# Performance work log

Hardware: AMD Instinct MI355X
Metric: run time of the kernel (lower is better)

## Reference

```python
import jax, jax.numpy as jnp
import numpy as np

B, C, T = 64, 22, 2560
U0, U1 = 128, 64  # lstm units per direction


def _lstm(x, Wx, Wh, b, reverse):
    """Keras-style LSTM. x:[B,T,D]. Returns (seq:[B,T,U], last:[B,U])."""
    if reverse:
        x = x[:, ::-1, :]
    U = Wh.shape[0]
    # precompute input projections for all timesteps: [T,B,4U]
    xz = (jnp.einsum('btd,dk->btk', x, Wx) + b).transpose(1, 0, 2)
    h0 = jnp.zeros((x.shape[0], U), x.dtype)
    c0 = jnp.zeros((x.shape[0], U), x.dtype)

    def step(carry, z):
        h, c = carry
        z = z + h @ Wh
        i = jax.nn.sigmoid(z[:, :U])
        f = jax.nn.sigmoid(z[:, U:2 * U])
        g = jnp.tanh(z[:, 2 * U:3 * U])
        o = jax.nn.sigmoid(z[:, 3 * U:])
        c = f * c + i * g
        h = o * jnp.tanh(c)
        return (h, c), h

    (h_last, _), hs = jax.lax.scan(step, (h0, c0), xz)
    hs = hs.transpose(1, 0, 2)  # [B,T,U]
    if reverse:
        hs = hs[:, ::-1, :]
    return hs, h_last


def setup_inputs() -> dict:
    key = jax.random.key(0)
    ks = jax.random.split(key, 20)
    s = 0.05
    d = {"x": jax.random.normal(ks[0], (B, C, T), jnp.float32)}
    # layer 0 (input dim C=22, units U0), fwd + bwd
    d["l0f_Wx"] = jax.random.normal(ks[1], (C, 4 * U0)) * s
    d["l0f_Wh"] = jax.random.normal(ks[2], (U0, 4 * U0)) * s
    d["l0f_b"] = jnp.zeros((4 * U0,))
    d["l0b_Wx"] = jax.random.normal(ks[3], (C, 4 * U0)) * s
    d["l0b_Wh"] = jax.random.normal(ks[4], (U0, 4 * U0)) * s
    d["l0b_b"] = jnp.zeros((4 * U0,))
    # layer 1 (input dim 2*U0=256, units U1), fwd + bwd
    d["l1f_Wx"] = jax.random.normal(ks[5], (2 * U0, 4 * U1)) * s
    d["l1f_Wh"] = jax.random.normal(ks[6], (U1, 4 * U1)) * s
    d["l1f_b"] = jnp.zeros((4 * U1,))
    d["l1b_Wx"] = jax.random.normal(ks[7], (2 * U0, 4 * U1)) * s
    d["l1b_Wh"] = jax.random.normal(ks[8], (U1, 4 * U1)) * s
    d["l1b_b"] = jnp.zeros((4 * U1,))
    # dense head: 2*U1=128 -> 128 -> 64 -> 1
    d["d0_W"] = jax.random.normal(ks[9], (2 * U1, 128)) * s
    d["d0_b"] = jnp.zeros((128,))
    d["d1_W"] = jax.random.normal(ks[10], (128, 64)) * s
    d["d1_b"] = jnp.zeros((64,))
    d["out_W"] = jax.random.normal(ks[11], (64, 1)) * s
    d["out_b"] = jnp.zeros((1,))
    return d


def reference(x, l0f_Wx, l0f_Wh, l0f_b, l0b_Wx, l0b_Wh, l0b_b,
              l1f_Wx, l1f_Wh, l1f_b, l1b_Wx, l1b_Wh, l1b_b,
              d0_W, d0_b, d1_W, d1_b, out_W, out_b):
    h = x.transpose(0, 2, 1)  # [B,T,C]
    # BiLSTM 0, return_sequences=True
    f_seq, _ = _lstm(h, l0f_Wx, l0f_Wh, l0f_b, reverse=False)
    b_seq, _ = _lstm(h, l0b_Wx, l0b_Wh, l0b_b, reverse=True)
    h = jnp.concatenate([f_seq, b_seq], axis=-1)  # [B,T,2*U0]
    # BiLSTM 1, return last state
    _, f_last = _lstm(h, l1f_Wx, l1f_Wh, l1f_b, reverse=False)
    _, b_last = _lstm(h, l1b_Wx, l1b_Wh, l1b_b, reverse=True)
    h = jnp.concatenate([f_last, b_last], axis=-1)  # [B,2*U1]
    # dense head (dropout inactive at inference)
    h = jax.nn.relu(h @ d0_W + d0_b)
    h = jax.nn.relu(h @ d1_W + d1_b)
    return jax.nn.sigmoid(h @ out_W + out_b)  # [B,1]
```

## Files before the change

kernel.cpp:

```cpp
#include <hip/hip_runtime.h>
#include <stdint.h>

#define TT 2560
#define BB 64
#define CC 22

typedef unsigned short ushort_t;
typedef __attribute__((ext_vector_type(4))) float floatx4;
typedef __attribute__((ext_vector_type(8))) short bf16x8;
typedef __attribute__((ext_vector_type(4))) int intx4;

__device__ __forceinline__ float bf2f(ushort_t u){
  union { uint32_t i; float f; } v; v.i = ((uint32_t)u) << 16; return v.f;
}
__device__ __forceinline__ ushort_t f2bf(float f){
  union { float f; uint32_t i; } v; v.f = f;
  uint32_t r = v.i + 0x7FFFu + ((v.i >> 16) & 1u);
  return (ushort_t)(r >> 16);
}
__device__ __forceinline__ float fsig(float x){ return 1.f/(1.f + __expf(-x)); }
__device__ __forceinline__ float ftanh(float x){ return 2.f/(1.f + __expf(-2.f*x)) - 1.f; }

__device__ __forceinline__ void ldsbar(){
  asm volatile("s_waitcnt lgkmcnt(0)\n\ts_barrier" ::: "memory");
}

__global__ __launch_bounds__(256) void k_convert_x(const float* __restrict__ x, ushort_t* __restrict__ xc){
  int i4 = blockIdx.x*256 + threadIdx.x;
  if (i4 >= BB*CC*TT/4) return;
  const float4 v = ((const float4*)x)[i4];
  uint2 o;
  o.x = (uint32_t)f2bf(v.x) | ((uint32_t)f2bf(v.y) << 16);
  o.y = (uint32_t)f2bf(v.z) | ((uint32_t)f2bf(v.w) << 16);
  ((uint2*)xc)[i4] = o;
}

__global__ __launch_bounds__(256) void k_prep_xa(const ushort_t* __restrict__ xc, ushort_t* __restrict__ xA){
  int idx = blockIdx.x*256 + threadIdx.x;
  if (idx >= BB*TT*4) return;
  int q = idx & 3;
  int rest = idx >> 2;
  int t = rest % TT, b = rest / TT;
  ushort_t v[8];
  #pragma unroll
  for (int j=0;j<8;j++){
    int c = q*8 + j;
    v[j] = (c < CC) ? xc[((size_t)b*CC + c)*TT + t] : (ushort_t)0;
  }
  *(uint4*)(xA + (size_t)idx*8) = *(const uint4*)v;
}

__global__ __launch_bounds__(256) void k_wmax(const float* __restrict__ w0f, const float* __restrict__ w0b,
                                              const float* __restrict__ w1f, const float* __restrict__ w1b,
                                              float* __restrict__ scl){
  const int b = blockIdx.x;
  const float* W = (b==0) ? w0f : (b==1) ? w0b : (b==2) ? w1f : w1b;
  const int n = (b < 2) ? 128*512 : 64*256;
  float mx = 0.f;
  for (int i = threadIdx.x; i < n; i += 256) mx = fmaxf(mx, fabsf(W[i]));
  __shared__ float red[256];
  red[threadIdx.x] = mx;
  __syncthreads();
  for (int s = 128; s > 0; s >>= 1){
    if (threadIdx.x < s) red[threadIdx.x] = fmaxf(red[threadIdx.x], red[threadIdx.x+s]);
    __syncthreads();
  }
  if (threadIdx.x == 0) scl[b] = fmaxf(red[0], 1e-8f);
}

__global__ __launch_bounds__(256) void k_prep_l0(const float* __restrict__ WxF, const float* __restrict__ WhF,
                                                 const float* __restrict__ WxB, const float* __restrict__ WhB,
                                                 const float* __restrict__ scl,
                                                 char* __restrict__ W0Q, ushort_t* __restrict__ B0X){
  int idx = blockIdx.x*256 + threadIdx.x;
  if (idx >= 2*512*160) return;
  int dir = idx / 81920; int r0 = idx % 81920; int n = r0 / 160; int k = r0 % 160;
  int g = n >> 7, u = n & 127;
  int wv = u >> 4, qq = (u >> 2) & 3, r = u & 3;
  int row = (qq*8 + wv)*16 + (r*4 + g);
  if (k < 128){
    const float* Wh = dir ? WhB : WhF;
    float sw = scl[dir];
    W0Q[(size_t)dir*65536 + row*128 + k] = (char)(int)rintf(Wh[k*512 + n] * (127.f/sw));
  } else {
    const float* Wx = dir ? WxB : WxF;
    int kx = k - 128;
    float v = (kx < CC) ? Wx[kx*512 + n] : 0.f;
    B0X[(size_t)dir*16384 + row*32 + kx] = f2bf(v);
  }
}

__global__ __launch_bounds__(256) void k_prep_l1(const float* __restrict__ WhF, const float* __restrict__ WhB,
                                                 const float* __restrict__ scl,
                                                 char* __restrict__ W1Q){
  int idx = blockIdx.x*256 + threadIdx.x;
  if (idx >= 2*256*64) return;
  int dir = idx >> 14; int r = idx & 16383; int n = r >> 6; int k = r & 63;
  const float* Wh = dir ? WhB : WhF;
  float sw = scl[2+dir];
  W1Q[(size_t)dir*16384 + n*64 + k] = (char)(int)rintf(Wh[k*256 + n] * (127.f/sw));
}

__global__ __launch_bounds__(256) void k_prep_wxT(const float* __restrict__ Wf, const float* __restrict__ Wb,
                                                  ushort_t* __restrict__ WT){
  int idx = blockIdx.x*256 + threadIdx.x;
  int dir = idx >> 16; int r = idx & 65535; int n = r >> 8; int k = r & 255;
  const float* W = dir ? Wb : Wf;
  WT[idx] = f2bf(W[k*256 + n]);
}

__global__ __launch_bounds__(512, 1) void k_lstm0m(
  const ushort_t* __restrict__ xA, const char* __restrict__ W0Q,
  const ushort_t* __restrict__ B0X, const float* __restrict__ scl,
  const float* __restrict__ bF, const float* __restrict__ bB,
  ushort_t* __restrict__ h0seq)
{
  const int dir = blockIdx.x & 1, b = blockIdx.x >> 1;
  const int tid = threadIdx.x;
  const int wv = tid >> 6, lane = tid & 63, m = lane & 15, q = lane >> 4;
  const int g  = m & 3;
  const int u  = wv*16 + q*4 + (m >> 2);
  const float* bi = dir ? bB : bF;
  const float sclc = scl[dir] * (1.f/16129.f);
  const float em = (g==2) ? -2.f : -1.f;
  const float ym = (g==2) ?  2.f :  1.f;
  const float ya = (g==2) ? -1.f :  0.f;
  const float bzl = bi[g*128 + u];

  __shared__ __align__(16) char AbufC[2][128];

  bf16x8 Bfx[4];
  intx4  BfQ[4][2];
  {
    const ushort_t* Bx = B0X + (size_t)dir*16384;
    const char*     Bq = W0Q + (size_t)dir*65536;
    #pragma unroll
    for (int qt=0; qt<4; qt++){
      int nrow = (qt*8 + wv)*16 + m;
      Bfx[qt] = *(const bf16x8*)(Bx + (size_t)nrow*32 + q*8);
      #pragma unroll
      for (int kt=0; kt<2; kt++)
        BfQ[qt][kt] = *(const intx4*)(Bq + (size_t)nrow*128 + kt*64 + q*16);
    }
  }

  if (tid < 64) ((uint32_t*)AbufC)[tid] = 0u;

  const ushort_t* xap = xA + ((size_t)b*TT*4 + q)*8;
  uint4 px[4];
  #pragma unroll
  for (int j=0; j<4; j++){
    int tj = dir ? (TT-1-j) : j;
    px[j] = *(const uint4*)(xap + (size_t)tj*32);
  }
  const ushort_t* xpp = xap + (size_t)(dir ? (TT-5) : 4)*32;
  const int xstep = dir ? -32 : 32;
  __syncthreads();

  const floatx4 z4 = {0.f,0.f,0.f,0.f};
  const intx4  zi = {0,0,0,0};
  float cst = 0.f;
  const int t00 = dir ? TT-1 : 0;
  ushort_t* hp = h0seq + ((size_t)b*TT + t00)*256 + dir*128 + u;
  const int hstep = dir ? -256 : 256;

  for (int i = 0; i < TT/4; ++i){
    #pragma unroll
    for (int p = 0; p < 4; ++p){
      const int s = i*4 + p;
      const int cur = s & 1, nxt = cur ^ 1;

      const char* ar = &AbufC[cur][0];
      intx4 AfQ0 = *(const intx4*)(ar + q*16);
      intx4 AfQ1 = *(const intx4*)(ar + 64 + q*16);
      bf16x8 Ax = *(const bf16x8*)&px[p];

      floatx4 ax0 = __builtin_amdgcn_mfma_f32_16x16x32_bf16(Ax, Bfx[0], z4, 0,0,0);
      floatx4 ax1 = __builtin_amdgcn_mfma_f32_16x16x32_bf16(Ax, Bfx[1], z4, 0,0,0);
      floatx4 ax2 = __builtin_amdgcn_mfma_f32_16x16x32_bf16(Ax, Bfx[2], z4, 0,0,0);
      floatx4 ax3 = __builtin_amdgcn_mfma_f32_16x16x32_bf16(Ax, Bfx[3], z4, 0,0,0);

      intx4 aq0 = __builtin_amdgcn_mfma_i32_16x16x64_i8(AfQ0, BfQ[0][0], zi, 0,0,0);
      intx4 aq1 = __builtin_amdgcn_mfma_i32_16x16x64_i8(AfQ0, BfQ[1][0], zi, 0,0,0);
      intx4 aq2 = __builtin_amdgcn_mfma_i32_16x16x64_i8(AfQ0, BfQ[2][0], zi, 0,0,0);
      intx4 aq3 = __builtin_amdgcn_mfma_i32_16x16x64_i8(AfQ0, BfQ[3][0], zi, 0,0,0);
      aq0 = __builtin_amdgcn_mfma_i32_16x16x64_i8(AfQ1, BfQ[0][1], aq0, 0,0,0);
      aq1 = __builtin_amdgcn_mfma_i32_16x16x64_i8(AfQ1, BfQ[1][1], aq1, 0,0,0);
      aq2 = __builtin_amdgcn_mfma_i32_16x16x64_i8(AfQ1, BfQ[2][1], aq2, 0,0,0);
      aq3 = __builtin_amdgcn_mfma_i32_16x16x64_i8(AfQ1, BfQ[3][1], aq3, 0,0,0);

      px[p] = *(const uint4*)xpp;
      xpp += xstep;

      float axs = (q < 2) ? ((q == 0) ? ax0[0] : ax1[0])
                          : ((q == 2) ? ax2[0] : ax3[0]);
      int   aqs = (q < 2) ? ((q == 0) ? aq0[0] : aq1[0])
                          : ((q == 2) ? aq2[0] : aq3[0]);

      {
        float z = (float)aqs*sclc + axs + bzl;
        float e = __expf(z * em);
        float y = 1.f/(1.f + e);
        float act = ym*y + ya;

        int ai = __float_as_int(act);
        float sf = __int_as_float(__builtin_amdgcn_ds_swizzle(ai, 0x041F));
        float sg = __int_as_float(__builtin_amdgcn_ds_swizzle(ai, 0x081F));
        float so = __int_as_float(__builtin_amdgcn_ds_swizzle(ai, 0x0C1F));

        float cc = sf*cst + act*sg;
        cst = cc;
        float hl = so*ftanh(cc);
        if (g == 0){
          AbufC[nxt][u] = (char)(int)rintf(hl * 127.f);
          *hp = f2bf(hl);
        }
        hp += hstep;
      }
      ldsbar();
    }
  }
}

__global__ __launch_bounds__(512) void k_xz1_gemm(const ushort_t* __restrict__ h0seq,
                                                  const ushort_t* __restrict__ WxT,
                                                  ushort_t* __restrict__ xz1)
{
  const int mb  = blockIdx.x;
  const int dir = blockIdx.y;
  const ushort_t* W   = WxT + (size_t)dir*256*256;
  ushort_t*       out = xz1 + (size_t)dir*BB*TT*256;
  const int wave = threadIdx.x >> 6;
  const int lane = threadIdx.x & 63;
  const int mw = wave & 3;
  const int nw = wave >> 2;
  const int m_ = lane & 15;
  const int q_ = lane >> 4;

  floatx4 acc[2][8];
  #pragma unroll
  for (int a=0;a<2;a++)
    #pragma unroll
    for (int n=0;n<8;n++) acc[a][n] = (floatx4)0.f;

  const size_t Abase = ((size_t)mb*128 + mw*32 + m_)*256 + q_*8;
  const size_t Bbase = ((size_t)nw*128 + m_)*256 + q_*8;

  for (int kc = 0; kc < 256; kc += 32){
    bf16x8 afr[2];
    #pragma unroll
    for (int mt=0;mt<2;mt++)
      afr[mt] = *(const bf16x8*)(h0seq + Abase + (size_t)mt*16*256 + kc);
    #pragma unroll
    for (int nt=0;nt<8;nt++){
      bf16x8 bfr = *(const bf16x8*)(W + Bbase + (size_t)nt*16*256 + kc);
      #pragma unroll
      for (int mt=0;mt<2;mt++)
        acc[mt][nt] = __builtin_amdgcn_mfma_f32_16x16x32_bf16(afr[mt], bfr, acc[mt][nt], 0,0,0);
    }
  }
  #pragma unroll
  for (int mt=0;mt<2;mt++)
    #pragma unroll
    for (int r=0;r<4;r++){
      size_t bt = (size_t)mb*128 + mw*32 + mt*16 + q_*4 + r;
      ushort_t* rowp = out + bt*256;
      #pragma unroll
      for (int wvz=0; wvz<4; wvz++){
        uint32_t lo = f2bf(acc[mt][wvz][r]);
        uint32_t hi = f2bf(acc[mt][wvz+4][r]);
        *(uint32_t*)(rowp + (wvz*16+m_)*4 + 2*nw) = lo | (hi << 16);
      }
    }
}

__global__ __launch_bounds__(256, 1) void k_lstm1m(
  const ushort_t* __restrict__ xz1R,
  const char* __restrict__ W1Q,
  const float* __restrict__ scl,
  const float* __restrict__ bF, const float* __restrict__ bB,
  float* __restrict__ h1last)
{
  const int dir = blockIdx.x & 1, cb = blockIdx.x >> 1;
  const int tid = threadIdx.x;
  const int wv = tid >> 6, lane = tid & 63, m = lane & 15, q = lane >> 4;
  const int u = wv*16 + m;
  const float* bi = dir ? bB : bF;
  const float sclc = scl[2+dir] * (1.f/16129.f);

  __shared__ __align__(16) char HbufC[2][4][80];

  intx4 BfQ[4];
  {
    const char* Bq = W1Q + (size_t)dir*16384;
    #pragma unroll
    for (int g=0; g<4; g++){
      int nrow = (g*4 + wv)*16 + m;
      BfQ[g] = *(const intx4*)(Bq + (size_t)nrow*64 + q*16);
    }
  }
  float bz[4];
  #pragma unroll
  for (int g=0; g<4; g++) bz[g] = bi[g*64 + u];

  if (tid < (int)(sizeof(HbufC)/4)) ((uint32_t*)HbufC)[tid] = 0u;

  const ushort_t* xzr = xz1R + ((size_t)dir*BB + (size_t)(cb*4+q))*TT*256 + (size_t)u*4;
  uint2 pz[4];
  #pragma unroll
  for (int j=0; j<4; j++){
    int tj = dir ? (TT-1-j) : j;
    pz[j] = *(const uint2*)(xzr + (size_t)tj*256);
  }
  const ushort_t* xpp = xzr + (size_t)(dir ? (TT-5) : 4)*256;
  const int zstep = dir ? -256 : 256;
  __syncthreads();

  const intx4 zi = {0,0,0,0};
  float cst = 0.f, hl = 0.f;
  const int ch = m >> 2;

  for (int i = 0; i < TT/4; ++i){
    #pragma unroll
    for (int p = 0; p < 4; ++p){
      const int s = i*4 + p;
      const int cur = s & 1, nxt = cur ^ 1;

      intx4 AfQ = *(const intx4*)(&HbufC[cur][ch][0] + q*16);

      float w0 = bz[0] + bf2f((ushort_t)(pz[p].x & 0xffff));
      float w1 = bz[1] + bf2f((ushort_t)(pz[p].x >> 16));
      float w2 = bz[2] + bf2f((ushort_t)(pz[p].y & 0xffff));
      float w3 = bz[3] + bf2f((ushort_t)(pz[p].y >> 16));
      pz[p] = *(const uint2*)xpp;
      xpp += zstep;

      intx4 a0 = __builtin_amdgcn_mfma_i32_16x16x64_i8(AfQ, BfQ[0], zi, 0,0,0);
      intx4 a1 = __builtin_amdgcn_mfma_i32_16x16x64_i8(AfQ, BfQ[1], zi, 0,0,0);
      intx4 a2 = __builtin_amdgcn_mfma_i32_16x16x64_i8(AfQ, BfQ[2], zi, 0,0,0);
      intx4 a3 = __builtin_amdgcn_mfma_i32_16x16x64_i8(AfQ, BfQ[3], zi, 0,0,0);

      {
        float ig = fsig((float)a0[0]*sclc + w0);
        float fg = fsig((float)a1[0]*sclc + w1);
        float gg = ftanh((float)a2[0]*sclc + w2);
        float og = fsig((float)a3[0]*sclc + w3);
        float cc = fg*cst + ig*gg;
        cst = cc;
        hl = og*ftanh(cc);
        HbufC[nxt][q][u] = (char)(int)rintf(hl * 127.f);
      }
      ldsbar();
    }
  }
  h1last[(size_t)(cb*4 + q)*128 + dir*64 + u] = hl;
}

__global__ __launch_bounds__(128) void k_head(
  const float* __restrict__ h1last,
  const float* __restrict__ d0W, const float* __restrict__ d0b,
  const float* __restrict__ d1W, const float* __restrict__ d1b,
  const float* __restrict__ oW,  const float* __restrict__ ob,
  float* __restrict__ outp)
{
  const int b = blockIdx.x;
  const int j = threadIdx.x;
  __shared__ float v0[128], v1[128];
  v0[j] = h1last[b*128 + j];
  __syncthreads();
  float acc = d0b[j];
  #pragma unroll
  for (int k=0;k<128;k++) acc += v0[k]*d0W[k*128 + j];
  v1[j] = fmaxf(acc, 0.f);
  __syncthreads();
  if (j < 64){
    float a2 = d1b[j];
    #pragma unroll
    for (int k=0;k<128;k++) a2 += v1[k]*d1W[k*64 + j];
    float p = fmaxf(a2, 0.f) * oW[j];
    #pragma unroll
    for (int off=32; off>0; off>>=1) p += __shfl_down(p, off, 64);
    if (j == 0) outp[b] = 1.f/(1.f + __expf(-(p + ob[0])));
  }
}

extern "C" void kernel_launch(void* const* d_in, const int* in_sizes, int n_in,
                              void* d_out, int out_size, void* d_ws, size_t ws_size,
                              hipStream_t stream)
{
  const float* x     = (const float*)d_in[0];
  const float* l0fWx = (const float*)d_in[1];
  const float* l0fWh = (const float*)d_in[2];
  const float* l0fb  = (const float*)d_in[3];
  const float* l0bWx = (const float*)d_in[4];
  const float* l0bWh = (const float*)d_in[5];
  const float* l0bb  = (const float*)d_in[6];
  const float* l1fWx = (const float*)d_in[7];
  const float* l1fWh = (const float*)d_in[8];
  const float* l1fb  = (const float*)d_in[9];
  const float* l1bWx = (const float*)d_in[10];
  const float* l1bWh = (const float*)d_in[11];
  const float* l1bb  = (const float*)d_in[12];
  const float* d0W = (const float*)d_in[13];
  const float* d0b = (const float*)d_in[14];
  const float* d1W = (const float*)d_in[15];
  const float* d1b = (const float*)d_in[16];
  const float* oW  = (const float*)d_in[17];
  const float* ob  = (const float*)d_in[18];
  float* outp = (float*)d_out;

  char* ws = (char*)d_ws;
  const size_t OFF_XT  = 0;
  const size_t OFF_SCL = 7208960ull;
  const size_t OFF_H0  = OFF_XT  + 7864320ull;
  const size_t OFF_XZ  = OFF_H0  + 83886080ull;
  const size_t OFF_XA  = OFF_XZ;
  const size_t OFF_WT  = OFF_XZ  + 167772160ull;
  const size_t OFF_B0  = OFF_WT  + 262144ull;
  const size_t OFF_B0X = OFF_B0  + 131072ull;
  const size_t OFF_B1  = OFF_B0  + 327680ull;
  const size_t OFF_H1  = OFF_B1  + 65536ull;

  ushort_t* xc  = (ushort_t*)(ws + OFF_XT);
  float*    sclp= (float*)(ws + OFF_SCL);
  ushort_t* h0  = (ushort_t*)(ws + OFF_H0);
  ushort_t* xz1 = (ushort_t*)(ws + OFF_XZ);
  ushort_t* xA  = (ushort_t*)(ws + OFF_XA);
  ushort_t* WT  = (ushort_t*)(ws + OFF_WT);
  char*     W0Q = (char*)(ws + OFF_B0);
  ushort_t* B0X = (ushort_t*)(ws + OFF_B0X);
  char*     W1Q = (char*)(ws + OFF_B1);
  float*    h1l = (float*)(ws + OFF_H1);

  hipLaunchKernelGGL(k_convert_x,   dim3(3520), dim3(256), 0, stream, x, xc);
  hipLaunchKernelGGL(k_prep_xa,     dim3(2560), dim3(256), 0, stream, xc, xA);
  hipLaunchKernelGGL(k_wmax,        dim3(4),    dim3(256), 0, stream, l0fWh, l0bWh, l1fWh, l1bWh, sclp);
  hipLaunchKernelGGL(k_prep_l0,     dim3(640),  dim3(256), 0, stream, l0fWx, l0fWh, l0bWx, l0bWh, sclp, W0Q, B0X);
  hipLaunchKernelGGL(k_prep_l1,     dim3(128),  dim3(256), 0, stream, l1fWh, l1bWh, sclp, W1Q);
  hipLaunchKernelGGL(k_prep_wxT,    dim3(512),  dim3(256), 0, stream, l1fWx, l1bWx, WT);
  hipLaunchKernelGGL(k_lstm0m,      dim3(128),  dim3(512), 0, stream, xA, W0Q, B0X, sclp, l0fb, l0bb, h0);
  hipLaunchKernelGGL(k_xz1_gemm,    dim3(1280,2), dim3(512), 0, stream, h0, WT, xz1);
  hipLaunchKernelGGL(k_lstm1m,      dim3(32),   dim3(256), 0, stream, xz1, W1Q, sclp, l1fb, l1bb, h1l);
  hipLaunchKernelGGL(k_head,        dim3(64),   dim3(128), 0, stream,
                     h1l, d0W, d0b, d1W, d1b, oW, ob, outp);
}
```

Baseline: 2.131 ms.

## Split layer-1 LSTM to one batch per block with gate-parallel lanes and swizzle exchange

```diff
diff --git a/kernel.cpp b/kernel.cpp
--- a/kernel.cpp
+++ b/kernel.cpp
@@ -95,10 +95,13 @@
                                                  char* __restrict__ W1Q){
   int idx = blockIdx.x*256 + threadIdx.x;
   if (idx >= 2*256*64) return;
-  int dir = idx >> 14; int r = idx & 16383; int n = r >> 6; int k = r & 63;
+  int dir = idx >> 14; int r0 = idx & 16383; int n = r0 >> 6; int k = r0 & 63;
+  int g = n >> 6, u = n & 63;
+  int wv = u >> 4, qq = (u >> 2) & 3, r = u & 3;
+  int row = (qq*4 + wv)*16 + (r*4 + g);
   const float* Wh = dir ? WhB : WhF;
   float sw = scl[2+dir];
-  W1Q[(size_t)dir*16384 + n*64 + k] = (char)(int)rintf(Wh[k*256 + n] * (127.f/sw));
+  W1Q[(size_t)dir*16384 + row*64 + k] = (char)(int)rintf(Wh[k*256 + n] * (127.f/sw));
 }
 
 __global__ __launch_bounds__(256) void k_prep_wxT(const float* __restrict__ Wf, const float* __restrict__ Wb,
@@ -281,36 +284,36 @@
   const float* __restrict__ bF, const float* __restrict__ bB,
   float* __restrict__ h1last)
 {
-  const int dir = blockIdx.x & 1, cb = blockIdx.x >> 1;
+  const int dir = blockIdx.x & 1, b = blockIdx.x >> 1;
   const int tid = threadIdx.x;
   const int wv = tid >> 6, lane = tid & 63, m = lane & 15, q = lane >> 4;
-  const int u = wv*16 + m;
+  const int g = m & 3;
+  const int u = wv*16 + q*4 + (m >> 2);
   const float* bi = dir ? bB : bF;
   const float sclc = scl[2+dir] * (1.f/16129.f);
-
-  __shared__ __align__(16) char HbufC[2][4][80];
+  const float em = (g==2) ? -2.f : -1.f;
+  const float ym = (g==2) ?  2.f :  1.f;
+  const float ya = (g==2) ? -1.f :  0.f;
+  const float bzl = bi[g*64 + u];
+
+  __shared__ __align__(16) char HbufC[2][64];
 
   intx4 BfQ[4];
   {
     const char* Bq = W1Q + (size_t)dir*16384;
     #pragma unroll
-    for (int g=0; g<4; g++){
-      int nrow = (g*4 + wv)*16 + m;
-      BfQ[g] = *(const intx4*)(Bq + (size_t)nrow*64 + q*16);
-    }
-  }
-  float bz[4];
-  #pragma unroll
-  for (int g=0; g<4; g++) bz[g] = bi[g*64 + u];
-
-  if (tid < (int)(sizeof(HbufC)/4)) ((uint32_t*)HbufC)[tid] = 0u;
-
-  const ushort_t* xzr = xz1R + ((size_t)dir*BB + (size_t)(cb*4+q))*TT*256 + (size_t)u*4;
-  uint2 pz[4];
+    for (int qt=0; qt<4; qt++)
+      BfQ[qt] = *(const intx4*)(Bq + (size_t)((qt*4 + wv)*16 + m)*64 + q*16);
+  }
+
+  if (tid < 32) ((uint32_t*)HbufC)[tid] = 0u;
+
+  const ushort_t* xzr = xz1R + ((size_t)dir*BB + b)*TT*256 + (size_t)(u*4 + g);
+  ushort_t pz[4];
   #pragma unroll
   for (int j=0; j<4; j++){
     int tj = dir ? (TT-1-j) : j;
-    pz[j] = *(const uint2*)(xzr + (size_t)tj*256);
+    pz[j] = xzr[(size_t)tj*256];
   }
   const ushort_t* xpp = xzr + (size_t)(dir ? (TT-5) : 4)*256;
   const int zstep = dir ? -256 : 256;
@@ -318,7 +321,6 @@
 
   const intx4 zi = {0,0,0,0};
   float cst = 0.f, hl = 0.f;
-  const int ch = m >> 2;
 
   for (int i = 0; i < TT/4; ++i){
     #pragma unroll
@@ -326,34 +328,40 @@
       const int s = i*4 + p;
       const int cur = s & 1, nxt = cur ^ 1;
 
-      intx4 AfQ = *(const intx4*)(&HbufC[cur][ch][0] + q*16);
-
-      float w0 = bz[0] + bf2f((ushort_t)(pz[p].x & 0xffff));
-      float w1 = bz[1] + bf2f((ushort_t)(pz[p].x >> 16));
-      float w2 = bz[2] + bf2f((ushort_t)(pz[p].y & 0xffff));
-      float w3 = bz[3] + bf2f((ushort_t)(pz[p].y >> 16));
-      pz[p] = *(const uint2*)xpp;
+      intx4 AfQ = *(const intx4*)(&HbufC[cur][0] + q*16);
+
+      float w = bzl + bf2f(pz[p]);
+      pz[p] = *xpp;
       xpp += zstep;
 
-      intx4 a0 = __builtin_amdgcn_mfma_i32_16x16x64_i8(AfQ, BfQ[0], zi, 0,0,0);
-      intx4 a1 = __builtin_amdgcn_mfma_i32_16x16x64_i8(AfQ, BfQ[1], zi, 0,0,0);
-      intx4 a2 = __builtin_amdgcn_mfma_i32_16x16x64_i8(AfQ, BfQ[2], zi, 0,0,0);
-      intx4 a3 = __builtin_amdgcn_mfma_i32_16x16x64_i8(AfQ, BfQ[3], zi, 0,0,0);
+      intx4 c0 = __builtin_amdgcn_mfma_i32_16x16x64_i8(AfQ, BfQ[0], zi, 0,0,0);
+      intx4 c1 = __builtin_amdgcn_mfma_i32_16x16x64_i8(AfQ, BfQ[1], zi, 0,0,0);
+      intx4 c2 = __builtin_amdgcn_mfma_i32_16x16x64_i8(AfQ, BfQ[2], zi, 0,0,0);
+      intx4 c3 = __builtin_amdgcn_mfma_i32_16x16x64_i8(AfQ, BfQ[3], zi, 0,0,0);
+
+      int aqs = (q < 2) ? ((q == 0) ? c0[0] : c1[0])
+                        : ((q == 2) ? c2[0] : c3[0]);
 
       {
-        float ig = fsig((float)a0[0]*sclc + w0);
-        float fg = fsig((float)a1[0]*sclc + w1);
-        float gg = ftanh((float)a2[0]*sclc + w2);
-        float og = fsig((float)a3[0]*sclc + w3);
-        float cc = fg*cst + ig*gg;
+        float z = (float)aqs*sclc + w;
+        float e = __expf(z * em);
+        float y = 1.f/(1.f + e);
+        float act = ym*y + ya;
+
+        int ai = __float_as_int(act);
+        float sf = __int_as_float(__builtin_amdgcn_ds_swizzle(ai, 0x041F));
+        float sg = __int_as_float(__builtin_amdgcn_ds_swizzle(ai, 0x081F));
+        float so = __int_as_float(__builtin_amdgcn_ds_swizzle(ai, 0x0C1F));
+
+        float cc = sf*cst + act*sg;
         cst = cc;
-        hl = og*ftanh(cc);
-        HbufC[nxt][q][u] = (char)(int)rintf(hl * 127.f);
+        hl = so*ftanh(cc);
+        if (g == 0) HbufC[nxt][u] = (char)(int)rintf(hl * 127.f);
       }
       ldsbar();
     }
   }
-  h1last[(size_t)(cb*4 + q)*128 + dir*64 + u] = hl;
+  if (g == 0) h1last[(size_t)b*128 + dir*64 + u] = hl;
 }
 
 __global__ __launch_bounds__(128) void k_head(
@@ -440,7 +448,7 @@
   hipLaunchKernelGGL(k_prep_wxT,    dim3(512),  dim3(256), 0, stream, l1fWx, l1bWx, WT);
   hipLaunchKernelGGL(k_lstm0m,      dim3(128),  dim3(512), 0, stream, xA, W0Q, B0X, sclp, l0fb, l0bb, h0);
   hipLaunchKernelGGL(k_xz1_gemm,    dim3(1280,2), dim3(512), 0, stream, h0, WT, xz1);
-  hipLaunchKernelGGL(k_lstm1m,      dim3(32),   dim3(256), 0, stream, xz1, W1Q, sclp, l1fb, l1bb, h1l);
+  hipLaunchKernelGGL(k_lstm1m,      dim3(128),  dim3(256), 0, stream, xz1, W1Q, sclp, l1fb, l1bb, h1l);
   hipLaunchKernelGGL(k_head,        dim3(64),   dim3(128), 0, stream,
                      h1l, d0W, d0b, d1W, d1b, oW, ob, outp);
 }
```

After: 2.106 ms (median of 2 runs). Within noise of the previous version (-1.2%).

## Run layer-1 LSTM as one wave per sequence using sdot4 instead of MFMA

Applied to the files above, without the earlier changes.

```diff
diff --git a/kernel.cpp b/kernel.cpp
--- a/kernel.cpp
+++ b/kernel.cpp
@@ -23,6 +23,23 @@
 
 __device__ __forceinline__ void ldsbar(){
   asm volatile("s_waitcnt lgkmcnt(0)\n\ts_barrier" ::: "memory");
+}
+__device__ __forceinline__ void ldsfence(){
+  asm volatile("s_waitcnt lgkmcnt(0)" ::: "memory");
+}
+
+__device__ __forceinline__ int dot4(int a, int b, int acc){
+#if __has_builtin(__builtin_amdgcn_sdot4)
+  return __builtin_amdgcn_sdot4(a, b, acc, false);
+#else
+  #pragma unroll
+  for (int j=0;j<4;j++){
+    int av = (int)(char)(a >> (8*j));
+    int bv = (int)(char)(b >> (8*j));
+    acc += av*bv;
+  }
+  return acc;
+#endif
 }
 
 __global__ __launch_bounds__(256) void k_convert_x(const float* __restrict__ x, ushort_t* __restrict__ xc){
@@ -274,38 +291,36 @@
     }
 }
 
-__global__ __launch_bounds__(256, 1) void k_lstm1m(
+__global__ __launch_bounds__(64, 1) void k_lstm1m(
   const ushort_t* __restrict__ xz1R,
   const char* __restrict__ W1Q,
   const float* __restrict__ scl,
   const float* __restrict__ bF, const float* __restrict__ bB,
   float* __restrict__ h1last)
 {
-  const int dir = blockIdx.x & 1, cb = blockIdx.x >> 1;
-  const int tid = threadIdx.x;
-  const int wv = tid >> 6, lane = tid & 63, m = lane & 15, q = lane >> 4;
-  const int u = wv*16 + m;
+  const int dir = blockIdx.x & 1, b = blockIdx.x >> 1;
+  const int u = threadIdx.x;
   const float* bi = dir ? bB : bF;
   const float sclc = scl[2+dir] * (1.f/16129.f);
 
-  __shared__ __align__(16) char HbufC[2][4][80];
-
-  intx4 BfQ[4];
+  __shared__ __align__(16) char hbuf[64];
+
+  intx4 Wd[4][4];
   {
     const char* Bq = W1Q + (size_t)dir*16384;
     #pragma unroll
-    for (int g=0; g<4; g++){
-      int nrow = (g*4 + wv)*16 + m;
-      BfQ[g] = *(const intx4*)(Bq + (size_t)nrow*64 + q*16);
-    }
+    for (int g=0; g<4; g++)
+      #pragma unroll
+      for (int c=0; c<4; c++)
+        Wd[g][c] = *(const intx4*)(Bq + (size_t)(g*64 + u)*64 + c*16);
   }
   float bz[4];
   #pragma unroll
   for (int g=0; g<4; g++) bz[g] = bi[g*64 + u];
 
-  if (tid < (int)(sizeof(HbufC)/4)) ((uint32_t*)HbufC)[tid] = 0u;
-
-  const ushort_t* xzr = xz1R + ((size_t)dir*BB + (size_t)(cb*4+q))*TT*256 + (size_t)u*4;
+  if (u < 16) ((uint32_t*)hbuf)[u] = 0u;
+
+  const ushort_t* xzr = xz1R + ((size_t)dir*BB + b)*TT*256 + (size_t)u*4;
   uint2 pz[4];
   #pragma unroll
   for (int j=0; j<4; j++){
@@ -314,19 +329,17 @@
   }
   const ushort_t* xpp = xzr + (size_t)(dir ? (TT-5) : 4)*256;
   const int zstep = dir ? -256 : 256;
-  __syncthreads();
-
-  const intx4 zi = {0,0,0,0};
+  ldsfence();
+
   float cst = 0.f, hl = 0.f;
-  const int ch = m >> 2;
 
   for (int i = 0; i < TT/4; ++i){
     #pragma unroll
     for (int p = 0; p < 4; ++p){
-      const int s = i*4 + p;
-      const int cur = s & 1, nxt = cur ^ 1;
-
-      intx4 AfQ = *(const intx4*)(&HbufC[cur][ch][0] + q*16);
+      intx4 h0_ = ((const intx4*)hbuf)[0];
+      intx4 h1_ = ((const intx4*)hbuf)[1];
+      intx4 h2_ = ((const intx4*)hbuf)[2];
+      intx4 h3_ = ((const intx4*)hbuf)[3];
 
       float w0 = bz[0] + bf2f((ushort_t)(pz[p].x & 0xffff));
       float w1 = bz[1] + bf2f((ushort_t)(pz[p].x >> 16));
@@ -335,25 +348,35 @@
       pz[p] = *(const uint2*)xpp;
       xpp += zstep;
 
-      intx4 a0 = __builtin_amdgcn_mfma_i32_16x16x64_i8(AfQ, BfQ[0], zi, 0,0,0);
-      intx4 a1 = __builtin_amdgcn_mfma_i32_16x16x64_i8(AfQ, BfQ[1], zi, 0,0,0);
-      intx4 a2 = __builtin_amdgcn_mfma_i32_16x16x64_i8(AfQ, BfQ[2], zi, 0,0,0);
-      intx4 a3 = __builtin_amdgcn_mfma_i32_16x16x64_i8(AfQ, BfQ[3], zi, 0,0,0);
+      int acc[4];
+      #pragma unroll
+      for (int g=0; g<4; g++){
+        int e0 = 0, e1 = 0;
+        e0 = dot4(h0_[0], Wd[g][0][0], e0);  e1 = dot4(h0_[1], Wd[g][0][1], e1);
+        e0 = dot4(h0_[2], Wd[g][0][2], e0);  e1 = dot4(h0_[3], Wd[g][0][3], e1);
+        e0 = dot4(h1_[0], Wd[g][1][0], e0);  e1 = dot4(h1_[1], Wd[g][1][1], e1);
+        e0 = dot4(h1_[2], Wd[g][1][2], e0);  e1 = dot4(h1_[3], Wd[g][1][3], e1);
+        e0 = dot4(h2_[0], Wd[g][2][0], e0);  e1 = dot4(h2_[1], Wd[g][2][1], e1);
+        e0 = dot4(h2_[2], Wd[g][2][2], e0);  e1 = dot4(h2_[3], Wd[g][2][3], e1);
+        e0 = dot4(h3_[0], Wd[g][3][0], e0);  e1 = dot4(h3_[1], Wd[g][3][1], e1);
+        e0 = dot4(h3_[2], Wd[g][3][2], e0);  e1 = dot4(h3_[3], Wd[g][3][3], e1);
+        acc[g] = e0 + e1;
+      }
 
       {
-        float ig = fsig((float)a0[0]*sclc + w0);
-        float fg = fsig((float)a1[0]*sclc + w1);
-        float gg = ftanh((float)a2[0]*sclc + w2);
-        float og = fsig((float)a3[0]*sclc + w3);
+        float ig = fsig ((float)acc[0]*sclc + w0);
+        float fg = fsig ((float)acc[1]*sclc + w1);
+        float gg = ftanh((float)acc[2]*sclc + w2);
+        float og = fsig ((float)acc[3]*sclc + w3);
         float cc = fg*cst + ig*gg;
         cst = cc;
         hl = og*ftanh(cc);
-        HbufC[nxt][q][u] = (char)(int)rintf(hl * 127.f);
+        hbuf[u] = (char)(int)rintf(hl * 127.f);
       }
-      ldsbar();
+      ldsfence();
     }
   }
-  h1last[(size_t)(cb*4 + q)*128 + dir*64 + u] = hl;
+  h1last[(size_t)b*128 + dir*64 + u] = hl;
 }
 
 __global__ __launch_bounds__(128) void k_head(
@@ -440,7 +463,7 @@
   hipLaunchKernelGGL(k_prep_wxT,    dim3(512),  dim3(256), 0, stream, l1fWx, l1bWx, WT);
   hipLaunchKernelGGL(k_lstm0m,      dim3(128),  dim3(512), 0, stream, xA, W0Q, B0X, sclp, l0fb, l0bb, h0);
   hipLaunchKernelGGL(k_xz1_gemm,    dim3(1280,2), dim3(512), 0, stream, h0, WT, xz1);
-  hipLaunchKernelGGL(k_lstm1m,      dim3(32),   dim3(256), 0, stream, xz1, W1Q, sclp, l1fb, l1bb, h1l);
+  hipLaunchKernelGGL(k_lstm1m,      dim3(128),  dim3(64), 0, stream, xz1, W1Q, sclp, l1fb, l1bb, h1l);
   hipLaunchKernelGGL(k_head,        dim3(64),   dim3(128), 0, stream,
                      h1l, d0W, d0b, d1W, d1b, oW, ob, outp);
 }
```

New measurement: 2.299 ms. +7.9%, slower.
